# Kernel optimization log

Hardware: AMD Instinct MI355X
Metric: run time of the kernel (lower is better)

Reference implementation:

```python
import jax, jax.numpy as jnp
import numpy as np

TOP_K = 2
LB_COEF = 0.01


def setup_inputs() -> dict:
    key = jax.random.key(0)
    k1, k2 = jax.random.split(key)
    x = jax.random.normal(k1, (4, 8192, 2048), dtype=jnp.float32)
    # router weight, torch Linear layout [num_experts, d_model]
    W = jax.random.normal(k2, (64, 2048), dtype=jnp.float32) * (1.0 / np.sqrt(2048))
    return {"x": x, "W": W}


def reference(x, W):
    # logits: [B, S, E]
    logits = jnp.einsum('bsd,ed->bse', x, W)
    top_k_logits, top_k_indices = jax.lax.top_k(logits, TOP_K)
    top_k_probs = jax.nn.softmax(top_k_logits, axis=-1)
    router_probs = jax.nn.softmax(logits, axis=-1)
    expert_probs = router_probs.mean(axis=(0, 1))  # [E]
    lb_loss = LB_COEF * jnp.sum(expert_probs * jnp.log(expert_probs + 1e-8))
    return top_k_probs, top_k_indices, lb_loss
```

## Files before the change

kernel.cpp:

```cpp
#include <hip/hip_runtime.h>

#define BM 64
#define KC 64
#define DD 2048
#define EE 64
#define NROWS 32768
#define NTILES (DD / KC)

__global__ __launch_bounds__(256) void router_main(const float* __restrict__ x,
                                                   const float* __restrict__ W,
                                                   float* __restrict__ out,
                                                   float* __restrict__ accum) {
    __shared__ __align__(16) float smem[16384];

    const int t = threadIdx.x;
    const int l = t & 63;
    const int w = t >> 6;
    const int row0 = blockIdx.x * BM;

    const char* xc = (const char*)x;
    const char* wc = (const char*)W;

    unsigned gxb[4], gwb[4];
    int ldsb[4];
#pragma unroll
    for (int i = 0; i < 4; ++i) {
        const int row = i * 16 + w * 4 + (l >> 4);
        const int c   = (l & 15) ^ ((4 * i + w) & 15);
        gxb[i]  = (unsigned)((( (unsigned)(row0 + row) * DD ) + c * 4) * 4);
        gwb[i]  = (unsigned)((( (unsigned)row * DD ) + c * 4) * 4);
        ldsb[i] = i * 1024 + w * 256;
    }

#define STAGE(buf, tile) do {                                                          \
    const unsigned kof_ = (unsigned)(tile) * (KC * 4);                                 \
    float* bx_ = smem + (buf) * 8192;                                                  \
    float* bw_ = bx_ + 4096;                                                           \
    _Pragma("unroll")                                                                  \
    for (int i_ = 0; i_ < 4; ++i_) {                                                   \
        __builtin_amdgcn_global_load_lds(                                              \
            (const __attribute__((address_space(1))) void*)(xc + gxb[i_] + kof_),      \
            (__attribute__((address_space(3))) void*)(bx_ + ldsb[i_]), 16, 0, 0);      \
        __builtin_amdgcn_global_load_lds(                                              \
            (const __attribute__((address_space(1))) void*)(wc + gwb[i_] + kof_),      \
            (__attribute__((address_space(3))) void*)(bw_ + ldsb[i_]), 16, 0, 0);      \
    }                                                                                  \
} while (0)

    const int tr = t & 15;
    const int tc = t >> 4;
    const int trm = tr << 2;
    const int tcm = tc << 2;

    float acc[4][4] = {};

    int cur = 0;
    STAGE(0, 0);
    __syncthreads();

    for (int tile = 0; tile < NTILES; ++tile) {
        if (tile + 1 < NTILES) STAGE(cur ^ 1, tile + 1);

        const float* bx = smem + cur * 8192;
        const float* bw = bx + 4096;
#pragma unroll
        for (int k4 = 0; k4 < 16; ++k4) {
            const int xo = trm ^ (k4 << 2);
            const int wo = tcm ^ (k4 << 2);
            float4 xa[4], wv[4];
#pragma unroll
            for (int i = 0; i < 4; ++i)
                xa[i] = *reinterpret_cast<const float4*>(bx + ((4 * tr + i) << 6) + xo);
#pragma unroll
            for (int j = 0; j < 4; ++j)
                wv[j] = *reinterpret_cast<const float4*>(bw + ((4 * tc + j) << 6) + wo);
#pragma unroll
            for (int i = 0; i < 4; ++i)
#pragma unroll
                for (int j = 0; j < 4; ++j) {
                    acc[i][j] = fmaf(xa[i].x, wv[j].x, acc[i][j]);
                    acc[i][j] = fmaf(xa[i].y, wv[j].y, acc[i][j]);
                    acc[i][j] = fmaf(xa[i].z, wv[j].z, acc[i][j]);
                    acc[i][j] = fmaf(xa[i].w, wv[j].w, acc[i][j]);
                }
        }
        __syncthreads();
        cur ^= 1;
    }

    float* lg     = smem;
    float* pm1    = smem + 4160;
    float* pi1    = smem + 4416;
    float* pm2    = smem + 4672;
    float* pi2    = smem + 4928;
    float* rowm   = smem + 5184;
    float* ps     = smem + 5248;
    float* rowinv = smem + 5504;
    float* cpart  = smem + 5568;

#pragma unroll
    for (int i = 0; i < 4; ++i)
#pragma unroll
        for (int j = 0; j < 4; ++j)
            lg[(4 * tr + i) * 65 + 4 * tc + j] = acc[i][j];
    __syncthreads();

    {
        const int q = t >> 6, r = t & 63;
        float m1 = -INFINITY, m2 = -INFINITY, i1 = 0.f, i2 = 0.f;
        const float* rowp = lg + r * 65 + q * 16;
        for (int e = 0; e < 16; ++e) {
            const float v = rowp[e];
            if (v > m1)      { m2 = m1; i2 = i1; m1 = v; i1 = (float)(q * 16 + e); }
            else if (v > m2) { m2 = v; i2 = (float)(q * 16 + e); }
        }
        pm1[q * 64 + r] = m1; pi1[q * 64 + r] = i1;
        pm2[q * 64 + r] = m2; pi2[q * 64 + r] = i2;
    }
    __syncthreads();

    if (t < 64) {
        const int r = t;
        float m1 = pm1[r], m2 = pm2[r], i1 = pi1[r], i2 = pi2[r];
        for (int q = 1; q < 4; ++q) {
            const float b1 = pm1[q * 64 + r], b2 = pm2[q * 64 + r];
            const float bi1 = pi1[q * 64 + r], bi2 = pi2[q * 64 + r];
            if (b1 > m1) {
                if (m1 >= b2) { m2 = m1; i2 = i1; }
                else          { m2 = b2; i2 = bi2; }
                m1 = b1; i1 = bi1;
            } else if (b1 > m2) { m2 = b1; i2 = bi1; }
        }
        rowm[r] = m1;
        const float e2  = __expf(m2 - m1);
        const float inv = 1.0f / (1.0f + e2);
        const size_t gr = (size_t)row0 + r;
        out[2 * gr]     = inv;
        out[2 * gr + 1] = e2 * inv;
        out[2 * (size_t)NROWS + 2 * gr]     = i1;
        out[2 * (size_t)NROWS + 2 * gr + 1] = i2;
    }
    __syncthreads();

    {
        const int q = t >> 6, r = t & 63;
        const float m = rowm[r];
        float s = 0.f;
        float* rowp = lg + r * 65 + q * 16;
        for (int e = 0; e < 16; ++e) {
            const float p = __expf(rowp[e] - m);
            rowp[e] = p;
            s += p;
        }
        ps[q * 64 + r] = s;
    }
    __syncthreads();

    if (t < 64) rowinv[t] = 1.0f / (ps[t] + ps[64 + t] + ps[128 + t] + ps[192 + t]);
    __syncthreads();

    {
        const int e = t & 63, q = t >> 6;
        float cs = 0.f;
        for (int rr = q * 16; rr < q * 16 + 16; ++rr)
            cs += lg[rr * 65 + e] * rowinv[rr];
        cpart[q * 64 + e] = cs;
    }
    __syncthreads();

    if (t < 64)
        atomicAdd(&accum[t], cpart[t] + cpart[64 + t] + cpart[128 + t] + cpart[192 + t]);
#undef STAGE
}

__global__ void router_loss(const float* __restrict__ accum, float* __restrict__ out) {
    const int e = threadIdx.x;
    const float p = accum[e] * (1.0f / (float)NROWS);
    float v = p * __logf(p + 1e-8f);
#pragma unroll
    for (int off = 32; off > 0; off >>= 1) v += __shfl_down(v, off);
    if (e == 0) out[4 * (size_t)NROWS] = 0.01f * v;
}

extern "C" void kernel_launch(void* const* d_in, const int* in_sizes, int n_in,
                              void* d_out, int out_size, void* d_ws, size_t ws_size,
                              hipStream_t stream) {
    const float* x = (const float*)d_in[0];
    const float* W = (const float*)d_in[1];
    float* out = (float*)d_out;
    float* accum = (float*)d_ws;

    hipMemsetAsync(d_ws, 0, EE * sizeof(float), stream);
    router_main<<<NROWS / BM, 256, 0, stream>>>(x, W, out, accum);
    router_loss<<<1, 64, 0, stream>>>(accum, out);
}
```

Measured before the change: 423.4 us.

## Use 128-row blocks with 8x8 register tiles and split-K across thread quads

```diff
diff --git a/kernel.cpp b/kernel.cpp
--- a/kernel.cpp
+++ b/kernel.cpp
@@ -1,83 +1,86 @@
 #include <hip/hip_runtime.h>
 
-#define BM 64
-#define KC 64
 #define DD 2048
 #define EE 64
 #define NROWS 32768
-#define NTILES (DD / KC)
-
-__global__ __launch_bounds__(256) void router_main(const float* __restrict__ x,
-                                                   const float* __restrict__ W,
-                                                   float* __restrict__ out,
-                                                   float* __restrict__ accum) {
-    __shared__ __align__(16) float smem[16384];
-
-    const int t = threadIdx.x;
-    const int l = t & 63;
-    const int w = t >> 6;
-    const int row0 = blockIdx.x * BM;
+#define BR 128
+#define ROUNDS 64
+
+__global__ __launch_bounds__(512, 2) void router_main(const float* __restrict__ x,
+                                                      const float* __restrict__ W,
+                                                      float* __restrict__ out,
+                                                      float* __restrict__ accum) {
+    __shared__ __align__(16) float smem[12288];
+
+    const int t  = threadIdx.x;
+    const int kq = t & 3;
+    const int eg = (t >> 2) & 7;
+    const int rg = t >> 5;
+    const int row0 = blockIdx.x * BR;
 
     const char* xc = (const char*)x;
     const char* wc = (const char*)W;
 
-    unsigned gxb[4], gwb[4];
-    int ldsb[4];
-#pragma unroll
-    for (int i = 0; i < 4; ++i) {
-        const int row = i * 16 + w * 4 + (l >> 4);
-        const int c   = (l & 15) ^ ((4 * i + w) & 15);
-        gxb[i]  = (unsigned)((( (unsigned)(row0 + row) * DD ) + c * 4) * 4);
-        gwb[i]  = (unsigned)((( (unsigned)row * DD ) + c * 4) * 4);
-        ldsb[i] = i * 1024 + w * 256;
-    }
-
-#define STAGE(buf, tile) do {                                                          \
-    const unsigned kof_ = (unsigned)(tile) * (KC * 4);                                 \
-    float* bx_ = smem + (buf) * 8192;                                                  \
-    float* bw_ = bx_ + 4096;                                                           \
+    unsigned gx[2]; int dx[2];
+#pragma unroll
+    for (int i = 0; i < 2; ++i) {
+        const int n = i * 512 + t;
+        const int row = n >> 3, p = n & 7;
+        const int c = p ^ ((n >> 6) & 7);
+        const unsigned col = (unsigned)((c >> 1) * 512 + (c & 1) * 4);
+        gx[i] = (unsigned)(((unsigned)(row0 + row) * DD + col) * 4);
+        dx[i] = n * 4;
+    }
+    unsigned gw; int dw;
+    {
+        const int n = t;
+        const int e = n >> 3, p = n & 7;
+        const int c = p ^ ((n >> 6) & 7);
+        const unsigned col = (unsigned)((c >> 1) * 512 + (c & 1) * 4);
+        gw = (unsigned)(((unsigned)e * DD + col) * 4);
+        dw = n * 4;
+    }
+
+#define STAGE(buf, round) do {                                                         \
+    const unsigned ro_ = (unsigned)(round) * 32u;              \
+    float* bb_ = smem + (buf) * 6144;                                                  \
     _Pragma("unroll")                                                                  \
-    for (int i_ = 0; i_ < 4; ++i_) {                                                   \
+    for (int i_ = 0; i_ < 2; ++i_)                                                     \
         __builtin_amdgcn_global_load_lds(                                              \
-            (const __attribute__((address_space(1))) void*)(xc + gxb[i_] + kof_),      \
-            (__attribute__((address_space(3))) void*)(bx_ + ldsb[i_]), 16, 0, 0);      \
-        __builtin_amdgcn_global_load_lds(                                              \
-            (const __attribute__((address_space(1))) void*)(wc + gwb[i_] + kof_),      \
-            (__attribute__((address_space(3))) void*)(bw_ + ldsb[i_]), 16, 0, 0);      \
-    }                                                                                  \
+            (const __attribute__((address_space(1))) void*)(xc + gx[i_] + ro_),        \
+            (__attribute__((address_space(3))) void*)(bb_ + dx[i_]), 16, 0, 0);        \
+    __builtin_amdgcn_global_load_lds(                                                  \
+        (const __attribute__((address_space(1))) void*)(wc + gw + ro_),                \
+        (__attribute__((address_space(3))) void*)(bb_ + 4096 + dw), 16, 0, 0);         \
 } while (0)
 
-    const int tr = t & 15;
-    const int tc = t >> 4;
-    const int trm = tr << 2;
-    const int tcm = tc << 2;
-
-    float acc[4][4] = {};
+    float acc[8][8];
+#pragma unroll
+    for (int i = 0; i < 8; ++i)
+#pragma unroll
+        for (int j = 0; j < 8; ++j) acc[i][j] = 0.f;
 
     int cur = 0;
     STAGE(0, 0);
     __syncthreads();
 
-    for (int tile = 0; tile < NTILES; ++tile) {
-        if (tile + 1 < NTILES) STAGE(cur ^ 1, tile + 1);
-
-        const float* bx = smem + cur * 8192;
-        const float* bw = bx + 4096;
-#pragma unroll
-        for (int k4 = 0; k4 < 16; ++k4) {
-            const int xo = trm ^ (k4 << 2);
-            const int wo = tcm ^ (k4 << 2);
-            float4 xa[4], wv[4];
-#pragma unroll
-            for (int i = 0; i < 4; ++i)
-                xa[i] = *reinterpret_cast<const float4*>(bx + ((4 * tr + i) << 6) + xo);
-#pragma unroll
-            for (int j = 0; j < 4; ++j)
-                wv[j] = *reinterpret_cast<const float4*>(bw + ((4 * tc + j) << 6) + wo);
-#pragma unroll
-            for (int i = 0; i < 4; ++i)
-#pragma unroll
-                for (int j = 0; j < 4; ++j) {
+    for (int round = 0; round < ROUNDS; ++round) {
+        if (round + 1 < ROUNDS) STAGE(cur ^ 1, round + 1);
+        const float4* bx = (const float4*)(smem + cur * 6144);
+        const float4* bw = (const float4*)(smem + cur * 6144 + 4096);
+#pragma unroll
+        for (int k4 = 0; k4 < 2; ++k4) {
+            const int px = (kq * 2 + k4) ^ (rg & 7);
+            const int pw = (kq * 2 + k4) ^ eg;
+            float4 xa[8], wv[8];
+#pragma unroll
+            for (int i = 0; i < 8; ++i) xa[i] = bx[(rg * 8 + i) * 8 + px];
+#pragma unroll
+            for (int j = 0; j < 8; ++j) wv[j] = bw[(eg * 8 + j) * 8 + pw];
+#pragma unroll
+            for (int i = 0; i < 8; ++i)
+#pragma unroll
+                for (int j = 0; j < 8; ++j) {
                     acc[i][j] = fmaf(xa[i].x, wv[j].x, acc[i][j]);
                     acc[i][j] = fmaf(xa[i].y, wv[j].y, acc[i][j]);
                     acc[i][j] = fmaf(xa[i].z, wv[j].z, acc[i][j]);
@@ -87,26 +90,39 @@
         __syncthreads();
         cur ^= 1;
     }
-
-    float* lg     = smem;
-    float* pm1    = smem + 4160;
-    float* pi1    = smem + 4416;
-    float* pm2    = smem + 4672;
-    float* pi2    = smem + 4928;
-    float* rowm   = smem + 5184;
-    float* ps     = smem + 5248;
-    float* rowinv = smem + 5504;
-    float* cpart  = smem + 5568;
-
-#pragma unroll
-    for (int i = 0; i < 4; ++i)
-#pragma unroll
-        for (int j = 0; j < 4; ++j)
-            lg[(4 * tr + i) * 65 + 4 * tc + j] = acc[i][j];
-    __syncthreads();
-
-    {
-        const int q = t >> 6, r = t & 63;
+#undef STAGE
+
+    float* lg = smem;
+    if (kq == 0) {
+#pragma unroll
+        for (int i = 0; i < 8; ++i)
+#pragma unroll
+            for (int j = 0; j < 8; ++j)
+                lg[(rg * 8 + i) * 65 + eg * 8 + j] = acc[i][j];
+    }
+    __syncthreads();
+    for (int q = 1; q < 4; ++q) {
+        if (kq == q) {
+#pragma unroll
+            for (int i = 0; i < 8; ++i)
+#pragma unroll
+                for (int j = 0; j < 8; ++j)
+                    lg[(rg * 8 + i) * 65 + eg * 8 + j] += acc[i][j];
+        }
+        __syncthreads();
+    }
+
+    float* pm1    = smem + 8320;
+    float* pi1    = smem + 8832;
+    float* pm2    = smem + 9344;
+    float* pi2    = smem + 9856;
+    float* rowm   = smem + 10368;
+    float* ps     = smem + 10496;
+    float* rowinv = smem + 11008;
+    float* cpart  = smem + 11136;
+
+    {
+        const int q = t >> 7, r = t & 127;
         float m1 = -INFINITY, m2 = -INFINITY, i1 = 0.f, i2 = 0.f;
         const float* rowp = lg + r * 65 + q * 16;
         for (int e = 0; e < 16; ++e) {
@@ -114,17 +130,17 @@
             if (v > m1)      { m2 = m1; i2 = i1; m1 = v; i1 = (float)(q * 16 + e); }
             else if (v > m2) { m2 = v; i2 = (float)(q * 16 + e); }
         }
-        pm1[q * 64 + r] = m1; pi1[q * 64 + r] = i1;
-        pm2[q * 64 + r] = m2; pi2[q * 64 + r] = i2;
-    }
-    __syncthreads();
-
-    if (t < 64) {
+        pm1[q * 128 + r] = m1; pi1[q * 128 + r] = i1;
+        pm2[q * 128 + r] = m2; pi2[q * 128 + r] = i2;
+    }
+    __syncthreads();
+
+    if (t < 128) {
         const int r = t;
         float m1 = pm1[r], m2 = pm2[r], i1 = pi1[r], i2 = pi2[r];
         for (int q = 1; q < 4; ++q) {
-            const float b1 = pm1[q * 64 + r], b2 = pm2[q * 64 + r];
-            const float bi1 = pi1[q * 64 + r], bi2 = pi2[q * 64 + r];
+            const float b1 = pm1[q * 128 + r], b2 = pm2[q * 128 + r];
+            const float bi1 = pi1[q * 128 + r], bi2 = pi2[q * 128 + r];
             if (b1 > m1) {
                 if (m1 >= b2) { m2 = m1; i2 = i1; }
                 else          { m2 = b2; i2 = bi2; }
@@ -143,7 +159,7 @@
     __syncthreads();
 
     {
-        const int q = t >> 6, r = t & 63;
+        const int q = t >> 7, r = t & 127;
         const float m = rowm[r];
         float s = 0.f;
         float* rowp = lg + r * 65 + q * 16;
@@ -152,11 +168,12 @@
             rowp[e] = p;
             s += p;
         }
-        ps[q * 64 + r] = s;
-    }
-    __syncthreads();
-
-    if (t < 64) rowinv[t] = 1.0f / (ps[t] + ps[64 + t] + ps[128 + t] + ps[192 + t]);
+        ps[q * 128 + r] = s;
+    }
+    __syncthreads();
+
+    if (t < 128)
+        rowinv[t] = 1.0f / (ps[t] + ps[128 + t] + ps[256 + t] + ps[384 + t]);
     __syncthreads();
 
     {
@@ -168,9 +185,12 @@
     }
     __syncthreads();
 
-    if (t < 64)
-        atomicAdd(&accum[t], cpart[t] + cpart[64 + t] + cpart[128 + t] + cpart[192 + t]);
-#undef STAGE
+    if (t < 64) {
+        float s = 0.f;
+#pragma unroll
+        for (int q = 0; q < 8; ++q) s += cpart[q * 64 + t];
+        atomicAdd(&accum[t], s);
+    }
 }
 
 __global__ void router_loss(const float* __restrict__ accum, float* __restrict__ out) {
@@ -191,6 +211,6 @@
     float* accum = (float*)d_ws;
 
     hipMemsetAsync(d_ws, 0, EE * sizeof(float), stream);
-    router_main<<<NROWS / BM, 256, 0, stream>>>(x, W, out, accum);
+    router_main<<<NROWS / BR, 512, 0, stream>>>(x, W, out, accum);
     router_loss<<<1, 64, 0, stream>>>(accum, out);
 }
```

Measured after the change: 453.6 us. 1.07x slower.
